# Performance work log

Measured on AMD Instinct MI355X. Metric: run time of the kernel, lower is better.

The kernel has to match this reference:

```python
import jax, jax.numpy as jnp
import numpy as np

B, S, H, NH = 2, 2048, 1024, 16
HD = H // NH  # head_size = 64


def setup_inputs() -> dict:
    key = jax.random.key(0)
    ks = jax.random.split(key, 9)
    sc = 0.02
    return {
        "hidden_states": jax.random.normal(ks[0], (B, S, H), dtype=jnp.float32),
        "Wq": jax.random.normal(ks[1], (H, H), dtype=jnp.float32) * sc,
        "bq": jax.random.normal(ks[2], (H,), dtype=jnp.float32) * sc,
        "Wk": jax.random.normal(ks[3], (H, H), dtype=jnp.float32) * sc,
        "bk": jax.random.normal(ks[4], (H,), dtype=jnp.float32) * sc,
        "Wv": jax.random.normal(ks[5], (H, H), dtype=jnp.float32) * sc,
        "bv": jax.random.normal(ks[6], (H,), dtype=jnp.float32) * sc,
        "Wo": jax.random.normal(ks[7], (H, H), dtype=jnp.float32) * sc,
        "bo": jax.random.normal(ks[8], (H,), dtype=jnp.float32) * sc,
    }


def reference(hidden_states, Wq, bq, Wk, bk, Wv, bv, Wo, bo):
    b, s, h = hidden_states.shape
    # nn.Linear: y = x @ W.T + b
    q = hidden_states @ Wq.T + bq
    k = hidden_states @ Wk.T + bk
    v = hidden_states @ Wv.T + bv
    q = q.reshape(b, s, NH, HD)
    k = k.reshape(b, s, NH, HD)
    v = v.reshape(b, s, NH, HD)
    # scores: [b, heads, q, k]
    scores = jnp.einsum("bqhd,bkhd->bhqk", q, k) / jnp.sqrt(jnp.float32(HD))
    # causal mask: triu(ones, diagonal=1) positions set to -inf
    causal = jnp.triu(jnp.ones((s, s), dtype=bool), k=1)
    scores = jnp.where(causal[None, None], -jnp.inf, scores)
    attn = jax.nn.softmax(scores, axis=-1)
    ctx = jnp.einsum("bhqk,bkhd->bqhd", attn, v).reshape(b, s, h)
    return ctx @ Wo.T + bo
```

## Files before the change

kernel.cpp:

```cpp
#include <hip/hip_runtime.h>
#include <hip/hip_bf16.h>

#define B_  2
#define S_  2048
#define H_  1024
#define NH_ 16
#define HD_ 64

typedef unsigned short u16;
typedef unsigned int   u32;
typedef __attribute__((ext_vector_type(4)))  float  f32x4;
typedef __attribute__((ext_vector_type(16))) float  f32x16;
typedef __attribute__((ext_vector_type(8)))  __bf16 bf16x8;
typedef __attribute__((ext_vector_type(2)))  unsigned int u32x2;
typedef __attribute__((ext_vector_type(4)))  unsigned int u32x4;
typedef __attribute__((ext_vector_type(4)))  unsigned short u16x4;

__device__ __forceinline__ u16 f2bf(float f) {
  unsigned u = __builtin_bit_cast(unsigned, f);
  u += 0x7fffu + ((u >> 16) & 1u);
  return (u16)(u >> 16);
}
__device__ __forceinline__ u32 cvtpk(float lo, float hi) {
  u32 r;
  asm("v_cvt_pk_bf16_f32 %0, %1, %2" : "=v"(r) : "v"(lo), "v"(hi));
  return r;
}
__device__ __forceinline__ float ex2(float x) {
  float r;
  asm("v_exp_f32 %0, %1" : "=v"(r) : "v"(x));
  return r;
}

__device__ __forceinline__ void gload_lds16(const void* g, void* l) {
  __builtin_amdgcn_global_load_lds(
      (const __attribute__((address_space(1))) void*)g,
      (__attribute__((address_space(3))) void*)l, 16, 0, 0);
}

#define NX_ (4u * 1024u * 1024u)
__global__ __launch_bounds__(256) void cvt_all(const float* __restrict__ x,
                                               const float* __restrict__ w0, const float* __restrict__ w1,
                                               const float* __restrict__ w2, const float* __restrict__ w3,
                                               u16* __restrict__ xb,
                                               u16* __restrict__ o0, u16* __restrict__ o1,
                                               u16* __restrict__ o2, u16* __restrict__ o3) {
  size_t i4 = ((size_t)blockIdx.x * 256 + threadIdx.x) * 4;
  const float* src; u16* dst; size_t off;
  if (i4 < (size_t)NX_) { src = x; dst = xb; off = i4; }
  else {
    size_t j = i4 - NX_;
    int seg = (int)(j >> 20);
    off = j & ((1u << 20) - 1);
    src = seg == 0 ? w0 : seg == 1 ? w1 : seg == 2 ? w2 : w3;
    dst = seg == 0 ? o0 : seg == 1 ? o1 : seg == 2 ? o2 : o3;
  }
  float4 v = *reinterpret_cast<const float4*>(src + off);
  u16x4 o;
  o[0] = f2bf(v.x); o[1] = f2bf(v.y); o[2] = f2bf(v.z); o[3] = f2bf(v.w);
  *reinterpret_cast<u16x4*>(dst + off) = o;
}

__device__ __forceinline__ void store_out(float* C, size_t idx, float v) { C[idx] = v; }
__device__ __forceinline__ void store_out(u16* C, size_t idx, float v) { C[idx] = f2bf(v); }

template <int MI, typename OutT>
__device__ __forceinline__ void gemm_core(const u16* __restrict__ A, const u16* __restrict__ Bw,
                                          const float* __restrict__ bias, OutT* __restrict__ C,
                                          int M, int N, int K, float oscale, int m0, int n0,
                                          u16* lsA, u16* lsB) {
  const int t = threadIdx.x;
  const int w = t >> 6, lane = t & 63;
  const int g = lane >> 4, c = lane & 15;
  const int wr = w >> 1, wc = w & 1;

  f32x4 acc[MI][4] = {};
  const int rowS = w * 16 + (lane >> 2);
  const int colS = (lane & 3) * 8;

  for (int k0 = 0; k0 < K; k0 += 32) {
    __syncthreads();
#pragma unroll
    for (int r = 0; r < MI / 2; ++r)
      gload_lds16(A + (size_t)(m0 + r * 64 + rowS) * K + k0 + colS, lsA + r * 2048 + w * 512);
#pragma unroll
    for (int r = 0; r < 2; ++r)
      gload_lds16(Bw + (size_t)(n0 + r * 64 + rowS) * K + k0 + colS, lsB + r * 2048 + w * 512);
    asm volatile("s_waitcnt vmcnt(0)" ::: "memory");
    __syncthreads();

    bf16x8 af[MI], bfr[4];
#pragma unroll
    for (int mi = 0; mi < MI; ++mi)
      af[mi] = *reinterpret_cast<const bf16x8*>(&lsA[(wr * (MI * 16) + mi * 16 + c) * 32 + g * 8]);
#pragma unroll
    for (int ni = 0; ni < 4; ++ni)
      bfr[ni] = *reinterpret_cast<const bf16x8*>(&lsB[(wc * 64 + ni * 16 + c) * 32 + g * 8]);
#pragma unroll
    for (int mi = 0; mi < MI; ++mi)
#pragma unroll
      for (int ni = 0; ni < 4; ++ni)
        acc[mi][ni] = __builtin_amdgcn_mfma_f32_16x16x32_bf16(af[mi], bfr[ni], acc[mi][ni], 0, 0, 0);
  }

#pragma unroll
  for (int mi = 0; mi < MI; ++mi) {
    int rowb = m0 + wr * (MI * 16) + mi * 16 + g * 4;
#pragma unroll
    for (int ni = 0; ni < 4; ++ni) {
      int col = n0 + wc * 64 + ni * 16 + c;
      float bv = bias[col];
#pragma unroll
      for (int r = 0; r < 4; ++r) {
        float v = (acc[mi][ni][r] + bv) * oscale;
        store_out(C, (size_t)(rowb + r) * N + col, v);
      }
    }
  }
}

__global__ __launch_bounds__(256) void gemm_qkv(const u16* __restrict__ xb,
                                                const u16* __restrict__ Wq, const u16* __restrict__ Wk,
                                                const u16* __restrict__ Wv,
                                                const float* __restrict__ bq, const float* __restrict__ bk,
                                                const float* __restrict__ bv,
                                                u16* __restrict__ Q, u16* __restrict__ Kb, u16* __restrict__ Vb,
                                                int M, int K, float qscale) {
  __shared__ u16 lsA[4096];
  __shared__ u16 lsB[4096];
  const int fid = blockIdx.x;
  const int xcd = fid & 7, i = fid >> 3;
  const int mloc = i / 24, nn = i % 24;
  const int m0 = (xcd * 4 + mloc) * 128;
  const int ng = nn * 128;
  const int sel = ng >> 10, n0 = ng & 1023;
  const u16*  W    = sel == 0 ? Wq : sel == 1 ? Wk : Wv;
  const float* bia = sel == 0 ? bq : sel == 1 ? bk : bv;
  u16*        Cp   = sel == 0 ? Q  : sel == 1 ? Kb : Vb;
  float os = sel == 0 ? qscale : 1.0f;
  gemm_core<4, u16>(xb, W, bia, Cp, M, 1024, K, os, m0, n0, lsA, lsB);
}

__global__ __launch_bounds__(256) void gemm_wo(const u16* __restrict__ A, const u16* __restrict__ Bw,
                                               const float* __restrict__ bias, float* __restrict__ C,
                                               int M, int N, int K) {
  __shared__ u16 lsA[2048];
  __shared__ u16 lsB[4096];
  const int fid = blockIdx.x;
  const int xcd = fid & 7, i = fid >> 3;
  const int mloc = i >> 3, nn = i & 7;
  const int m0 = (xcd * 8 + mloc) * 64;
  const int n0 = nn * 128;
  gemm_core<2, float>(A, Bw, bias, C, M, N, K, 1.0f, m0, n0, lsA, lsB);
}

__device__ __forceinline__ void stage_k(const u16* __restrict__ Kg, size_t headoff, int kvb,
                                        int kRow0, int kColB, int w, u16* lsKbuf) {
#pragma unroll
  for (int r = 0; r < 2; ++r)
    gload_lds16((const char*)(Kg + headoff + (size_t)(kvb + r * 32 + kRow0) * H_) + kColB,
                (char*)lsKbuf + r * 4096 + w * 1024);
}

__device__ __forceinline__ void write_vt(u16* dst, const u32x2* va, const u32x2* vb,
                                         int vKv, int vD0, int vS) {
#pragma unroll
  for (int r = 0; r < 2; ++r) {
    int kvx = (r * 32 + vKv) ^ vS;
    u32 w0 = __builtin_amdgcn_perm(vb[r][0], va[r][0], 0x05040100u);
    u32 w1 = __builtin_amdgcn_perm(vb[r][0], va[r][0], 0x07060302u);
    u32 w2 = __builtin_amdgcn_perm(vb[r][1], va[r][1], 0x05040100u);
    u32 w3 = __builtin_amdgcn_perm(vb[r][1], va[r][1], 0x07060302u);
    *reinterpret_cast<u32*>(dst + (vD0 + 0) * 72 + kvx) = w0;
    *reinterpret_cast<u32*>(dst + (vD0 + 1) * 72 + kvx) = w1;
    *reinterpret_cast<u32*>(dst + (vD0 + 2) * 72 + kvx) = w2;
    *reinterpret_cast<u32*>(dst + (vD0 + 3) * 72 + kvx) = w3;
  }
}

__device__ __forceinline__ void pv_sub(const f32x16& sc, float mrun, int ktbase,
                                       const char* vtb, int hi, int c5,
                                       f32x16& o0, f32x16& o1, float& rs) {
  float p[16];
#pragma unroll
  for (int r = 0; r < 16; ++r) p[r] = ex2(sc[r] - mrun);
  rs += ((p[0] + p[1]) + (p[2] + p[3])) + ((p[4] + p[5]) + (p[6] + p[7]))
      + ((p[8] + p[9]) + (p[10] + p[11])) + ((p[12] + p[13]) + (p[14] + p[15]));
  u32 wd[4][2];
#pragma unroll
  for (int a = 0; a < 4; ++a) {
    wd[a][0] = cvtpk(p[4 * a + 0], p[4 * a + 1]);
    wd[a][1] = cvtpk(p[4 * a + 2], p[4 * a + 3]);
  }
#pragma unroll
  for (int ktp = 0; ktp < 2; ++ktp) {
    u32 mw[4];
#pragma unroll
    for (int u = 0; u < 2; ++u) {
      u32 A  = wd[2 * ktp][u], Bv = wd[2 * ktp + 1][u];
      u32 oA = (u32)__shfl_xor((int)A, 32);
      u32 oB = (u32)__shfl_xor((int)Bv, 32);
      mw[u]     = hi ? oB : A;
      mw[2 + u] = hi ? Bv : oA;
    }
    u32x4 pw = {mw[0], mw[1], mw[2], mw[3]};
    bf16x8 pb = __builtin_bit_cast(bf16x8, pw);
    const int kt = ktbase + ktp;
#pragma unroll
    for (int dt = 0; dt < 2; ++dt) {
      int d = 32 * dt + c5;
      int col = (kt * 32 + hi * 16) ^ (16 * ((d >> 3) & 7));
      bf16x8 av = *reinterpret_cast<const bf16x8*>(vtb + d * 144 + col);
      f32x16& oo = dt ? o1 : o0;
      oo = __builtin_amdgcn_mfma_f32_32x32x16_bf16(av, pb, oo, 0, 0, 0);
    }
  }
}

__global__ __launch_bounds__(256, 4) void attn_fwd(const u16* __restrict__ Qg,
                                                   const u16* __restrict__ Kg,
                                                   const u16* __restrict__ Vg,
                                                   u16* __restrict__ Og) {
  __shared__ __align__(16) char smem[34816];
  u16* lsK  = (u16*)smem;
  u16* lsVt = (u16*)(smem + 16384);
  float* lsO  = (float*)smem;
  float* lsML = (float*)(smem + 20480);
  u16*   lsOT = (u16*)(smem + 21504);

  const int blk = blockIdx.x;
  const int xcd = blk & 7, i = blk >> 3;
  const int qt  = 31 - (i >> 2);
  const int bh  = xcd * 4 + (i & 3);
  const int h = bh & 15, b = bh >> 4;

  const int t = threadIdx.x, w = t >> 6, lane = t & 63;
  const int sub = w & 1, par = w >> 1;
  const int c5 = lane & 31, hi = lane >> 5;
  const size_t headoff = (size_t)b * (S_ * H_) + (size_t)h * HD_;
  const int q0w = qt * 64 + 32 * sub;

  const int kO    = w * 1024 + lane * 16;
  const int kRow0 = kO >> 7;
  const int kColB = (kO & 127) ^ ((kRow0 & 7) << 4);
  const int vKv = 2 * (t >> 4);
  const int vD0 = 4 * (t & 15);
  const int vS  = 8 * ((vD0 >> 3) & 7);

  bf16x8 aq[4];
#pragma unroll
  for (int kt = 0; kt < 4; ++kt)
    aq[kt] = *reinterpret_cast<const bf16x8*>(Qg + headoff + (size_t)(q0w + c5) * H_ + kt * 16 + hi * 8);

  f32x16 oacc0 = {}, oacc1 = {};
  float mrun = -1e30f, lrun = 0.f;

  const int NIT = (qt >> 1) + 1;
  for (int n = 0; n < NIT; ++n) {
    const int kvb0 = 2 * n * 64;
    const bool has1 = (2 * n + 1) <= qt;

    u32x2 va0[2], vb0[2], va1[2], vb1[2];
#pragma unroll
    for (int r = 0; r < 2; ++r) {
      const u16* vp = Vg + headoff + (size_t)(kvb0 + r * 32 + vKv) * H_ + vD0;
      va0[r] = *reinterpret_cast<const u32x2*>(vp);
      vb0[r] = *reinterpret_cast<const u32x2*>(vp + H_);
    }
    if (has1) {
#pragma unroll
      for (int r = 0; r < 2; ++r) {
        const u16* vp = Vg + headoff + (size_t)(kvb0 + 64 + r * 32 + vKv) * H_ + vD0;
        va1[r] = *reinterpret_cast<const u32x2*>(vp);
        vb1[r] = *reinterpret_cast<const u32x2*>(vp + H_);
      }
    }
    stage_k(Kg, headoff, kvb0, kRow0, kColB, w, lsK);
    if (has1) stage_k(Kg, headoff, kvb0 + 64, kRow0, kColB, w, lsK + 4096);
    asm volatile("s_waitcnt vmcnt(0)" ::: "memory");
    write_vt(lsVt, va0, vb0, vKv, vD0, vS);
    if (has1) write_vt(lsVt + 4608, va1, vb1, vKv, vD0, vS);
    __syncthreads();

    const int myt = 2 * n + par;
    if (myt <= qt) {
      const char* kb  = (const char*)lsK  + par * 8192;
      const char* vtb = (const char*)lsVt + par * 9216;
      const int nkv = (myt == qt && sub == 0) ? 1 : 2;

      f32x16 sc0 = {}, sc1 = {};
      __builtin_amdgcn_s_setprio(1);
#pragma unroll
      for (int kt = 0; kt < 4; ++kt) {
        int colx = (kt * 32 + hi * 16) ^ ((c5 & 7) << 4);
        bf16x8 ak0 = *reinterpret_cast<const bf16x8*>(kb + c5 * 128 + colx);
        sc0 = __builtin_amdgcn_mfma_f32_32x32x16_bf16(ak0, aq[kt], sc0, 0, 0, 0);
      }
      if (nkv == 2) {
#pragma unroll
        for (int kt = 0; kt < 4; ++kt) {
          int colx = (kt * 32 + hi * 16) ^ ((c5 & 7) << 4);
          bf16x8 ak1 = *reinterpret_cast<const bf16x8*>(kb + (32 + c5) * 128 + colx);
          sc1 = __builtin_amdgcn_mfma_f32_32x32x16_bf16(ak1, aq[kt], sc1, 0, 0, 0);
        }
      }
      __builtin_amdgcn_s_setprio(0);

      if (myt == qt) {
        const int qg = q0w + c5;
#pragma unroll
        for (int r = 0; r < 16; ++r) {
          int kvg = myt * 64 + (r & 3) + 8 * (r >> 2) + 4 * hi;
          sc0[r] = (kvg > qg) ? -1e30f : sc0[r];
          if (nkv == 2) sc1[r] = (kvg + 32 > qg) ? -1e30f : sc1[r];
        }
      }

      float pm = sc0[0];
#pragma unroll
      for (int r = 1; r < 16; ++r) pm = fmaxf(pm, sc0[r]);
      if (nkv == 2) {
#pragma unroll
        for (int r = 0; r < 16; ++r) pm = fmaxf(pm, sc1[r]);
      }
      pm = fmaxf(pm, (float)__shfl_xor(pm, 32));

      if (!__all(pm <= mrun + 8.0f)) {
        float mn = fmaxf(mrun, pm);
        float s8 = ex2(mrun - mn);
        mrun = mn; lrun *= s8;
#pragma unroll
        for (int r = 0; r < 16; ++r) { oacc0[r] *= s8; oacc1[r] *= s8; }
      }

      float rs = 0.f;
      pv_sub(sc0, mrun, 0, vtb, hi, c5, oacc0, oacc1, rs);
      if (nkv == 2) pv_sub(sc1, mrun, 2, vtb, hi, c5, oacc0, oacc1, rs);
      rs += (float)__shfl_xor(rs, 32);
      lrun += rs;
    }
    __syncthreads();
  }

  if (par == 0) {
    if (hi == 0) { lsML[sub * 64 + c5] = mrun; lsML[sub * 64 + 32 + c5] = lrun; }
#pragma unroll
    for (int dt = 0; dt < 2; ++dt) {
      float* dst = lsO + ((size_t)((sub * 2 + dt) * 64 + lane)) * 20;
      const f32x16& oo = dt ? oacc1 : oacc0;
#pragma unroll
      for (int k4 = 0; k4 < 4; ++k4) {
        f32x4 v4 = {oo[4 * k4], oo[4 * k4 + 1], oo[4 * k4 + 2], oo[4 * k4 + 3]};
        *reinterpret_cast<f32x4*>(dst + 4 * k4) = v4;
      }
    }
  }
  __syncthreads();
  if (par == 1) {
    float mA = lsML[sub * 64 + c5];
    float lA = lsML[sub * 64 + 32 + c5];
    float mn = fmaxf(mA, mrun);
    float sA = ex2(mA - mn), sB = ex2(mrun - mn);
    float linv = 1.0f / (lA * sA + lrun * sB);
    sA *= linv; sB *= linv;
    u16* ot = lsOT + sub * 32 * 72;
#pragma unroll
    for (int dt = 0; dt < 2; ++dt) {
      const float* sp = lsO + ((size_t)((sub * 2 + dt) * 64 + lane)) * 20;
      f32x4 a4[4];
#pragma unroll
      for (int k4 = 0; k4 < 4; ++k4) a4[k4] = *reinterpret_cast<const f32x4*>(sp + 4 * k4);
      const f32x16& oo = dt ? oacc1 : oacc0;
#pragma unroll
      for (int a = 0; a < 4; ++a)
#pragma unroll
        for (int u = 0; u < 2; ++u) {
          int r = 4 * a + 2 * u;
          float o0 = a4[a][2 * u]     * sA + oo[r]     * sB;
          float o1 = a4[a][2 * u + 1] * sA + oo[r + 1] * sB;
          int d = 32 * dt + 8 * a + 4 * hi + 2 * u;
          *reinterpret_cast<u32*>(ot + c5 * 72 + d) = cvtpk(o0, o1);
        }
    }
    asm volatile("s_waitcnt lgkmcnt(0)" ::: "memory");
    __builtin_amdgcn_sched_barrier(0);
#pragma unroll
    for (int rr = 0; rr < 4; ++rr) {
      int q = 8 * rr + (lane >> 3);
      int d8 = (lane & 7) * 8;
      u32x4 vv = *reinterpret_cast<const u32x4*>(ot + q * 72 + d8);
      *reinterpret_cast<u32x4*>(Og + headoff + (size_t)(qt * 64 + 32 * sub + q) * H_ + d8) = vv;
    }
  }
}

extern "C" void kernel_launch(void* const* d_in, const int* in_sizes, int n_in,
                              void* d_out, int out_size, void* d_ws, size_t ws_size,
                              hipStream_t stream) {
  const float* x  = (const float*)d_in[0];
  const float* Wq = (const float*)d_in[1];
  const float* bq = (const float*)d_in[2];
  const float* Wk = (const float*)d_in[3];
  const float* bk = (const float*)d_in[4];
  const float* Wv = (const float*)d_in[5];
  const float* bv = (const float*)d_in[6];
  const float* Wo = (const float*)d_in[7];
  const float* bo = (const float*)d_in[8];
  float* out = (float*)d_out;

  const size_t MT = (size_t)B_ * S_;
  char* p = (char*)d_ws;
  u16* xb  = (u16*)p; p += MT * H_ * 2;
  u16* Wqb = (u16*)p; p += (size_t)H_ * H_ * 2;
  u16* Wkb = (u16*)p; p += (size_t)H_ * H_ * 2;
  u16* Wvb = (u16*)p; p += (size_t)H_ * H_ * 2;
  u16* Wob = (u16*)p; p += (size_t)H_ * H_ * 2;
  u16* Qb  = (u16*)p; p += MT * H_ * 2;
  u16* Kb  = (u16*)p; p += MT * H_ * 2;
  u16* Vb  = (u16*)p; p += MT * H_ * 2;
  u16* Cb  = xb;

  cvt_all<<<8192, 256, 0, stream>>>(x, Wq, Wk, Wv, Wo, xb, Wqb, Wkb, Wvb, Wob);

  const float qscale = 0.125f * 1.44269504088896f;
  gemm_qkv<<<768, 256, 0, stream>>>(xb, Wqb, Wkb, Wvb, bq, bk, bv,
                                    Qb, Kb, Vb, (int)MT, H_, qscale);

  attn_fwd<<<1024, 256, 0, stream>>>(Qb, Kb, Vb, Cb);

  gemm_wo<<<512, 256, 0, stream>>>(Cb, Wob, bo, out, (int)MT, H_, H_);
}
```

Measured before the change: 113.2 us.

## Restructure attention to 128-query tiles with double-buffered K/V prefetch

```diff
diff --git a/kernel.cpp b/kernel.cpp
--- a/kernel.cpp
+++ b/kernel.cpp
@@ -162,6 +162,16 @@
                 (char*)lsKbuf + r * 4096 + w * 1024);
 }
 
+__device__ __forceinline__ void load_v(const u16* __restrict__ Vg, size_t headoff, int kvb,
+                                       int vKv, int vD0, u32x2* va, u32x2* vb) {
+#pragma unroll
+  for (int r = 0; r < 2; ++r) {
+    const u16* vp = Vg + headoff + (size_t)(kvb + r * 32 + vKv) * H_ + vD0;
+    va[r] = *reinterpret_cast<const u32x2*>(vp);
+    vb[r] = *reinterpret_cast<const u32x2*>(vp + H_);
+  }
+}
+
 __device__ __forceinline__ void write_vt(u16* dst, const u32x2* va, const u32x2* vb,
                                          int vKv, int vD0, int vS) {
 #pragma unroll
@@ -224,21 +234,21 @@
   __shared__ __align__(16) char smem[34816];
   u16* lsK  = (u16*)smem;
   u16* lsVt = (u16*)(smem + 16384);
-  float* lsO  = (float*)smem;
-  float* lsML = (float*)(smem + 20480);
-  u16*   lsOT = (u16*)(smem + 21504);
+  u16* lsOT = (u16*)smem;
 
   const int blk = blockIdx.x;
   const int xcd = blk & 7, i = blk >> 3;
-  const int qt  = 31 - (i >> 2);
+  const int qt  = 15 - (i >> 2);
   const int bh  = xcd * 4 + (i & 3);
   const int h = bh & 15, b = bh >> 4;
 
   const int t = threadIdx.x, w = t >> 6, lane = t & 63;
-  const int sub = w & 1, par = w >> 1;
   const int c5 = lane & 31, hi = lane >> 5;
   const size_t headoff = (size_t)b * (S_ * H_) + (size_t)h * HD_;
-  const int q0w = qt * 64 + 32 * sub;
+  const int q0w = qt * 128 + 32 * w;
+  const int NT  = 2 * qt + 2;
+  const int ktd = q0w >> 6;
+  const bool evenAligned = ((q0w & 63) == 0);
 
   const int kO    = w * 1024 + lane * 16;
   const int kRow0 = kO >> 7;
@@ -249,74 +259,60 @@
 
   bf16x8 aq[4];
 #pragma unroll
-  for (int kt = 0; kt < 4; ++kt)
-    aq[kt] = *reinterpret_cast<const bf16x8*>(Qg + headoff + (size_t)(q0w + c5) * H_ + kt * 16 + hi * 8);
+  for (int kc = 0; kc < 4; ++kc)
+    aq[kc] = *reinterpret_cast<const bf16x8*>(Qg + headoff + (size_t)(q0w + c5) * H_ + kc * 16 + hi * 8);
 
   f32x16 oacc0 = {}, oacc1 = {};
   float mrun = -1e30f, lrun = 0.f;
-
-  const int NIT = (qt >> 1) + 1;
-  for (int n = 0; n < NIT; ++n) {
-    const int kvb0 = 2 * n * 64;
-    const bool has1 = (2 * n + 1) <= qt;
-
-    u32x2 va0[2], vb0[2], va1[2], vb1[2];
-#pragma unroll
-    for (int r = 0; r < 2; ++r) {
-      const u16* vp = Vg + headoff + (size_t)(kvb0 + r * 32 + vKv) * H_ + vD0;
-      va0[r] = *reinterpret_cast<const u32x2*>(vp);
-      vb0[r] = *reinterpret_cast<const u32x2*>(vp + H_);
-    }
-    if (has1) {
-#pragma unroll
-      for (int r = 0; r < 2; ++r) {
-        const u16* vp = Vg + headoff + (size_t)(kvb0 + 64 + r * 32 + vKv) * H_ + vD0;
-        va1[r] = *reinterpret_cast<const u32x2*>(vp);
-        vb1[r] = *reinterpret_cast<const u32x2*>(vp + H_);
-      }
-    }
-    stage_k(Kg, headoff, kvb0, kRow0, kColB, w, lsK);
-    if (has1) stage_k(Kg, headoff, kvb0 + 64, kRow0, kColB, w, lsK + 4096);
-    asm volatile("s_waitcnt vmcnt(0)" ::: "memory");
-    write_vt(lsVt, va0, vb0, vKv, vD0, vS);
-    if (has1) write_vt(lsVt + 4608, va1, vb1, vKv, vD0, vS);
-    __syncthreads();
-
-    const int myt = 2 * n + par;
-    if (myt <= qt) {
-      const char* kb  = (const char*)lsK  + par * 8192;
-      const char* vtb = (const char*)lsVt + par * 9216;
-      const int nkv = (myt == qt && sub == 0) ? 1 : 2;
-
-      f32x16 sc0 = {}, sc1 = {};
+  u32x2 va[2], vb[2];
+
+  load_v(Vg, headoff, 0, vKv, vD0, va, vb);
+  stage_k(Kg, headoff, 0, kRow0, kColB, w, lsK);
+  asm volatile("s_waitcnt vmcnt(2)" ::: "memory");
+  write_vt(lsVt, va, vb, vKv, vD0, vS);
+  __syncthreads();
+
+  for (int it = 0; it < NT; ++it) {
+    const int cur = it & 1;
+    const bool st = (it + 1 < NT);
+    if (st) {
+      load_v(Vg, headoff, (it + 1) * 64, vKv, vD0, va, vb);
+      stage_k(Kg, headoff, (it + 1) * 64, kRow0, kColB, w, lsK + (cur ^ 1) * 4096);
+    }
+
+    const bool live = (it <= ktd);
+    const int nkv = (it == ktd && evenAligned) ? 1 : 2;
+    f32x16 sc0 = {}, sc1 = {};
+    float pm = -1e30f;
+    if (live) {
+      const char* kb = (const char*)(lsK + cur * 4096);
       __builtin_amdgcn_s_setprio(1);
 #pragma unroll
-      for (int kt = 0; kt < 4; ++kt) {
-        int colx = (kt * 32 + hi * 16) ^ ((c5 & 7) << 4);
+      for (int kc = 0; kc < 4; ++kc) {
+        int colx = (kc * 32 + hi * 16) ^ ((c5 & 7) << 4);
         bf16x8 ak0 = *reinterpret_cast<const bf16x8*>(kb + c5 * 128 + colx);
-        sc0 = __builtin_amdgcn_mfma_f32_32x32x16_bf16(ak0, aq[kt], sc0, 0, 0, 0);
+        sc0 = __builtin_amdgcn_mfma_f32_32x32x16_bf16(ak0, aq[kc], sc0, 0, 0, 0);
       }
       if (nkv == 2) {
 #pragma unroll
-        for (int kt = 0; kt < 4; ++kt) {
-          int colx = (kt * 32 + hi * 16) ^ ((c5 & 7) << 4);
+        for (int kc = 0; kc < 4; ++kc) {
+          int colx = (kc * 32 + hi * 16) ^ ((c5 & 7) << 4);
           bf16x8 ak1 = *reinterpret_cast<const bf16x8*>(kb + (32 + c5) * 128 + colx);
-          sc1 = __builtin_amdgcn_mfma_f32_32x32x16_bf16(ak1, aq[kt], sc1, 0, 0, 0);
+          sc1 = __builtin_amdgcn_mfma_f32_32x32x16_bf16(ak1, aq[kc], sc1, 0, 0, 0);
         }
       }
       __builtin_amdgcn_s_setprio(0);
 
-      if (myt == qt) {
-        const int qg = q0w + c5;
+      if (it == ktd) {
 #pragma unroll
         for (int r = 0; r < 16; ++r) {
-          int kvg = myt * 64 + (r & 3) + 8 * (r >> 2) + 4 * hi;
-          sc0[r] = (kvg > qg) ? -1e30f : sc0[r];
-          if (nkv == 2) sc1[r] = (kvg + 32 > qg) ? -1e30f : sc1[r];
+          int j = (r & 3) + 8 * (r >> 2) + 4 * hi;
+          if (evenAligned) sc0[r] = (j > c5) ? -1e30f : sc0[r];
+          else             sc1[r] = (j > c5) ? -1e30f : sc1[r];
         }
       }
 
-      float pm = sc0[0];
+      pm = sc0[0];
 #pragma unroll
       for (int r = 1; r < 16; ++r) pm = fmaxf(pm, sc0[r]);
       if (nkv == 2) {
@@ -332,65 +328,50 @@
 #pragma unroll
         for (int r = 0; r < 16; ++r) { oacc0[r] *= s8; oacc1[r] *= s8; }
       }
-
+    }
+
+    if (st) {
+      asm volatile("s_waitcnt vmcnt(2)" ::: "memory");
+      write_vt(lsVt + (cur ^ 1) * 4608, va, vb, vKv, vD0, vS);
+    }
+
+    if (live) {
+      const char* vtb = (const char*)(lsVt + cur * 4608);
       float rs = 0.f;
+      __builtin_amdgcn_s_setprio(1);
       pv_sub(sc0, mrun, 0, vtb, hi, c5, oacc0, oacc1, rs);
       if (nkv == 2) pv_sub(sc1, mrun, 2, vtb, hi, c5, oacc0, oacc1, rs);
+      __builtin_amdgcn_s_setprio(0);
       rs += (float)__shfl_xor(rs, 32);
       lrun += rs;
     }
+
     __syncthreads();
   }
 
-  if (par == 0) {
-    if (hi == 0) { lsML[sub * 64 + c5] = mrun; lsML[sub * 64 + 32 + c5] = lrun; }
-#pragma unroll
-    for (int dt = 0; dt < 2; ++dt) {
-      float* dst = lsO + ((size_t)((sub * 2 + dt) * 64 + lane)) * 20;
-      const f32x16& oo = dt ? oacc1 : oacc0;
-#pragma unroll
-      for (int k4 = 0; k4 < 4; ++k4) {
-        f32x4 v4 = {oo[4 * k4], oo[4 * k4 + 1], oo[4 * k4 + 2], oo[4 * k4 + 3]};
-        *reinterpret_cast<f32x4*>(dst + 4 * k4) = v4;
-      }
-    }
-  }
-  __syncthreads();
-  if (par == 1) {
-    float mA = lsML[sub * 64 + c5];
-    float lA = lsML[sub * 64 + 32 + c5];
-    float mn = fmaxf(mA, mrun);
-    float sA = ex2(mA - mn), sB = ex2(mrun - mn);
-    float linv = 1.0f / (lA * sA + lrun * sB);
-    sA *= linv; sB *= linv;
-    u16* ot = lsOT + sub * 32 * 72;
-#pragma unroll
-    for (int dt = 0; dt < 2; ++dt) {
-      const float* sp = lsO + ((size_t)((sub * 2 + dt) * 64 + lane)) * 20;
-      f32x4 a4[4];
-#pragma unroll
-      for (int k4 = 0; k4 < 4; ++k4) a4[k4] = *reinterpret_cast<const f32x4*>(sp + 4 * k4);
-      const f32x16& oo = dt ? oacc1 : oacc0;
-#pragma unroll
-      for (int a = 0; a < 4; ++a)
-#pragma unroll
-        for (int u = 0; u < 2; ++u) {
-          int r = 4 * a + 2 * u;
-          float o0 = a4[a][2 * u]     * sA + oo[r]     * sB;
-          float o1 = a4[a][2 * u + 1] * sA + oo[r + 1] * sB;
-          int d = 32 * dt + 8 * a + 4 * hi + 2 * u;
-          *reinterpret_cast<u32*>(ot + c5 * 72 + d) = cvtpk(o0, o1);
-        }
-    }
-    asm volatile("s_waitcnt lgkmcnt(0)" ::: "memory");
-    __builtin_amdgcn_sched_barrier(0);
-#pragma unroll
-    for (int rr = 0; rr < 4; ++rr) {
-      int q = 8 * rr + (lane >> 3);
-      int d8 = (lane & 7) * 8;
-      u32x4 vv = *reinterpret_cast<const u32x4*>(ot + q * 72 + d8);
-      *reinterpret_cast<u32x4*>(Og + headoff + (size_t)(qt * 64 + 32 * sub + q) * H_ + d8) = vv;
-    }
+  float linv = 1.0f / lrun;
+  u16* ot = lsOT + w * 2304;
+#pragma unroll
+  for (int dt = 0; dt < 2; ++dt) {
+    const f32x16& oo = dt ? oacc1 : oacc0;
+#pragma unroll
+    for (int a = 0; a < 4; ++a)
+#pragma unroll
+      for (int u = 0; u < 2; ++u) {
+        int r = 4 * a + 2 * u;
+        float o0 = oo[r] * linv, o1 = oo[r + 1] * linv;
+        int d = 32 * dt + 8 * a + 4 * hi + 2 * u;
+        *reinterpret_cast<u32*>(ot + c5 * 72 + d) = cvtpk(o0, o1);
+      }
+  }
+  asm volatile("s_waitcnt lgkmcnt(0)" ::: "memory");
+  __builtin_amdgcn_sched_barrier(0);
+#pragma unroll
+  for (int rr = 0; rr < 4; ++rr) {
+    int q = 8 * rr + (lane >> 3);
+    int d8 = (lane & 7) * 8;
+    u32x4 vv = *reinterpret_cast<const u32x4*>(ot + q * 72 + d8);
+    *reinterpret_cast<u32x4*>(Og + headoff + (size_t)(q0w + q) * H_ + d8) = vv;
   }
 }
 
@@ -426,7 +407,7 @@
   gemm_qkv<<<768, 256, 0, stream>>>(xb, Wqb, Wkb, Wvb, bq, bk, bv,
                                     Qb, Kb, Vb, (int)MT, H_, qscale);
 
-  attn_fwd<<<1024, 256, 0, stream>>>(Qb, Kb, Vb, Cb);
+  attn_fwd<<<512, 256, 0, stream>>>(Qb, Kb, Vb, Cb);
 
   gemm_wo<<<512, 256, 0, stream>>>(Cb, Wob, bo, out, (int)MT, H_, H_);
 }
```

After: 147.1 us. 29.9% more time.

## Double-buffer attention K/V tiles and deepen GEMM K-step to 64

Applied to the files above, without the earlier changes.

```diff
diff --git a/kernel.cpp b/kernel.cpp
--- a/kernel.cpp
+++ b/kernel.cpp
@@ -12,7 +12,6 @@
 typedef __attribute__((ext_vector_type(4)))  float  f32x4;
 typedef __attribute__((ext_vector_type(16))) float  f32x16;
 typedef __attribute__((ext_vector_type(8)))  __bf16 bf16x8;
-typedef __attribute__((ext_vector_type(2)))  unsigned int u32x2;
 typedef __attribute__((ext_vector_type(4)))  unsigned int u32x4;
 typedef __attribute__((ext_vector_type(4)))  unsigned short u16x4;
 
@@ -73,34 +72,45 @@
   const int w = t >> 6, lane = t & 63;
   const int g = lane >> 4, c = lane & 15;
   const int wr = w >> 1, wc = w & 1;
+  const int srow = lane >> 3;
+  const int scol = (lane & 7) * 8;
 
   f32x4 acc[MI][4] = {};
-  const int rowS = w * 16 + (lane >> 2);
-  const int colS = (lane & 3) * 8;
-
-  for (int k0 = 0; k0 < K; k0 += 32) {
+
+  for (int k0 = 0; k0 < K; k0 += 64) {
     __syncthreads();
 #pragma unroll
-    for (int r = 0; r < MI / 2; ++r)
-      gload_lds16(A + (size_t)(m0 + r * 64 + rowS) * K + k0 + colS, lsA + r * 2048 + w * 512);
-#pragma unroll
-    for (int r = 0; r < 2; ++r)
-      gload_lds16(Bw + (size_t)(n0 + r * 64 + rowS) * K + k0 + colS, lsB + r * 2048 + w * 512);
+    for (int j = 0; j < MI; ++j)
+      gload_lds16(A + (size_t)(m0 + 8 * (w * MI + j) + srow) * K + k0 + scol,
+                  lsA + 8 * (w * MI + j) * 64 + lane * 8);
+#pragma unroll
+    for (int j = 0; j < 4; ++j)
+      gload_lds16(Bw + (size_t)(n0 + 8 * (w * 4 + j) + srow) * K + k0 + scol,
+                  lsB + 8 * (w * 4 + j) * 64 + lane * 8);
     asm volatile("s_waitcnt vmcnt(0)" ::: "memory");
     __syncthreads();
 
-    bf16x8 af[MI], bfr[4];
+    bf16x8 af[MI][2], bfr[4][2];
 #pragma unroll
     for (int mi = 0; mi < MI; ++mi)
-      af[mi] = *reinterpret_cast<const bf16x8*>(&lsA[(wr * (MI * 16) + mi * 16 + c) * 32 + g * 8]);
+#pragma unroll
+      for (int kh = 0; kh < 2; ++kh)
+        af[mi][kh] = *reinterpret_cast<const bf16x8*>(
+            &lsA[(wr * (MI * 16) + mi * 16 + c) * 64 + kh * 32 + g * 8]);
 #pragma unroll
     for (int ni = 0; ni < 4; ++ni)
-      bfr[ni] = *reinterpret_cast<const bf16x8*>(&lsB[(wc * 64 + ni * 16 + c) * 32 + g * 8]);
-#pragma unroll
-    for (int mi = 0; mi < MI; ++mi)
-#pragma unroll
-      for (int ni = 0; ni < 4; ++ni)
-        acc[mi][ni] = __builtin_amdgcn_mfma_f32_16x16x32_bf16(af[mi], bfr[ni], acc[mi][ni], 0, 0, 0);
+#pragma unroll
+      for (int kh = 0; kh < 2; ++kh)
+        bfr[ni][kh] = *reinterpret_cast<const bf16x8*>(
+            &lsB[(wc * 64 + ni * 16 + c) * 64 + kh * 32 + g * 8]);
+#pragma unroll
+    for (int kh = 0; kh < 2; ++kh)
+#pragma unroll
+      for (int mi = 0; mi < MI; ++mi)
+#pragma unroll
+        for (int ni = 0; ni < 4; ++ni)
+          acc[mi][ni] = __builtin_amdgcn_mfma_f32_16x16x32_bf16(af[mi][kh], bfr[ni][kh],
+                                                                acc[mi][ni], 0, 0, 0);
   }
 
 #pragma unroll
@@ -126,8 +136,8 @@
                                                 const float* __restrict__ bv,
                                                 u16* __restrict__ Q, u16* __restrict__ Kb, u16* __restrict__ Vb,
                                                 int M, int K, float qscale) {
-  __shared__ u16 lsA[4096];
-  __shared__ u16 lsB[4096];
+  __shared__ u16 lsA[8192];
+  __shared__ u16 lsB[8192];
   const int fid = blockIdx.x;
   const int xcd = fid & 7, i = fid >> 3;
   const int mloc = i / 24, nn = i % 24;
@@ -144,8 +154,8 @@
 __global__ __launch_bounds__(256) void gemm_wo(const u16* __restrict__ A, const u16* __restrict__ Bw,
                                                const float* __restrict__ bias, float* __restrict__ C,
                                                int M, int N, int K) {
-  __shared__ u16 lsA[2048];
-  __shared__ u16 lsB[4096];
+  __shared__ u16 lsA[4096];
+  __shared__ u16 lsB[8192];
   const int fid = blockIdx.x;
   const int xcd = fid & 7, i = fid >> 3;
   const int mloc = i >> 3, nn = i & 7;
@@ -154,192 +164,167 @@
   gemm_core<2, float>(A, Bw, bias, C, M, N, K, 1.0f, m0, n0, lsA, lsB);
 }
 
-__device__ __forceinline__ void stage_k(const u16* __restrict__ Kg, size_t headoff, int kvb,
-                                        int kRow0, int kColB, int w, u16* lsKbuf) {
-#pragma unroll
-  for (int r = 0; r < 2; ++r)
-    gload_lds16((const char*)(Kg + headoff + (size_t)(kvb + r * 32 + kRow0) * H_) + kColB,
-                (char*)lsKbuf + r * 4096 + w * 1024);
-}
-
-__device__ __forceinline__ void write_vt(u16* dst, const u32x2* va, const u32x2* vb,
-                                         int vKv, int vD0, int vS) {
-#pragma unroll
-  for (int r = 0; r < 2; ++r) {
-    int kvx = (r * 32 + vKv) ^ vS;
-    u32 w0 = __builtin_amdgcn_perm(vb[r][0], va[r][0], 0x05040100u);
-    u32 w1 = __builtin_amdgcn_perm(vb[r][0], va[r][0], 0x07060302u);
-    u32 w2 = __builtin_amdgcn_perm(vb[r][1], va[r][1], 0x05040100u);
-    u32 w3 = __builtin_amdgcn_perm(vb[r][1], va[r][1], 0x07060302u);
-    *reinterpret_cast<u32*>(dst + (vD0 + 0) * 72 + kvx) = w0;
-    *reinterpret_cast<u32*>(dst + (vD0 + 1) * 72 + kvx) = w1;
-    *reinterpret_cast<u32*>(dst + (vD0 + 2) * 72 + kvx) = w2;
-    *reinterpret_cast<u32*>(dst + (vD0 + 3) * 72 + kvx) = w3;
-  }
-}
-
-__device__ __forceinline__ void pv_sub(const f32x16& sc, float mrun, int ktbase,
-                                       const char* vtb, int hi, int c5,
-                                       f32x16& o0, f32x16& o1, float& rs) {
-  float p[16];
-#pragma unroll
-  for (int r = 0; r < 16; ++r) p[r] = ex2(sc[r] - mrun);
-  rs += ((p[0] + p[1]) + (p[2] + p[3])) + ((p[4] + p[5]) + (p[6] + p[7]))
-      + ((p[8] + p[9]) + (p[10] + p[11])) + ((p[12] + p[13]) + (p[14] + p[15]));
-  u32 wd[4][2];
-#pragma unroll
-  for (int a = 0; a < 4; ++a) {
-    wd[a][0] = cvtpk(p[4 * a + 0], p[4 * a + 1]);
-    wd[a][1] = cvtpk(p[4 * a + 2], p[4 * a + 3]);
-  }
-#pragma unroll
-  for (int ktp = 0; ktp < 2; ++ktp) {
-    u32 mw[4];
-#pragma unroll
-    for (int u = 0; u < 2; ++u) {
-      u32 A  = wd[2 * ktp][u], Bv = wd[2 * ktp + 1][u];
-      u32 oA = (u32)__shfl_xor((int)A, 32);
-      u32 oB = (u32)__shfl_xor((int)Bv, 32);
-      mw[u]     = hi ? oB : A;
-      mw[2 + u] = hi ? Bv : oA;
-    }
-    u32x4 pw = {mw[0], mw[1], mw[2], mw[3]};
-    bf16x8 pb = __builtin_bit_cast(bf16x8, pw);
-    const int kt = ktbase + ktp;
-#pragma unroll
-    for (int dt = 0; dt < 2; ++dt) {
-      int d = 32 * dt + c5;
-      int col = (kt * 32 + hi * 16) ^ (16 * ((d >> 3) & 7));
-      bf16x8 av = *reinterpret_cast<const bf16x8*>(vtb + d * 144 + col);
-      f32x16& oo = dt ? o1 : o0;
-      oo = __builtin_amdgcn_mfma_f32_32x32x16_bf16(av, pb, oo, 0, 0, 0);
-    }
-  }
-}
-
 __global__ __launch_bounds__(256, 4) void attn_fwd(const u16* __restrict__ Qg,
                                                    const u16* __restrict__ Kg,
                                                    const u16* __restrict__ Vg,
                                                    u16* __restrict__ Og) {
-  __shared__ __align__(16) char smem[34816];
-  u16* lsK  = (u16*)smem;
-  u16* lsVt = (u16*)(smem + 16384);
+  __shared__ __align__(16) u16 smem[18432];
+  u16* lsKb = smem;
+  u16* lsVb = smem + 8192;
   float* lsO  = (float*)smem;
-  float* lsML = (float*)(smem + 20480);
-  u16*   lsOT = (u16*)(smem + 21504);
+  float* lsML = (float*)((char*)smem + 20480);
+  u16*   lsOT = smem + 10752;
 
   const int blk = blockIdx.x;
   const int xcd = blk & 7, i = blk >> 3;
-  const int qt  = 31 - (i >> 2);
-  const int bh  = xcd * 4 + (i & 3);
+  const int j5 = i & 31, bgrp = i >> 5;
+  const int qt = 31 - ((j5 + 8 * bgrp) & 31);
+  const int bh = xcd * 4 + bgrp;
   const int h = bh & 15, b = bh >> 4;
 
   const int t = threadIdx.x, w = t >> 6, lane = t & 63;
+  const int c5 = lane & 31, hi = lane >> 5;
   const int sub = w & 1, par = w >> 1;
-  const int c5 = lane & 31, hi = lane >> 5;
   const size_t headoff = (size_t)b * (S_ * H_) + (size_t)h * HD_;
   const int q0w = qt * 64 + 32 * sub;
 
-  const int kO    = w * 1024 + lane * 16;
-  const int kRow0 = kO >> 7;
-  const int kColB = (kO & 127) ^ ((kRow0 & 7) << 4);
-  const int vKv = 2 * (t >> 4);
-  const int vD0 = 4 * (t & 15);
-  const int vS  = 8 * ((vD0 >> 3) & 7);
+  const int sp = w & 1, sh = w >> 1;
+  const int kRowLoc = 16 * sh + (lane >> 3);
+  const int kSrcCol = ((lane & 7) ^ (lane >> 3)) << 4;
+  const int vKvLoc  = 16 * sh + 2 * (lane >> 3);
+  const int vD0     = 8 * (lane & 7);
+  const int vKvx    = vKvLoc ^ (((lane & 7) & 3) << 3);
+
+  int qkOff[4];
+#pragma unroll
+  for (int kc = 0; kc < 4; ++kc)
+    qkOff[kc] = c5 * 128 + ((32 * kc + 16 * hi) ^ ((c5 & 7) << 4));
+  const int pvRow0 = c5 * 80, pvRow1 = (32 + c5) * 80;
+  int pvCol[2];
+#pragma unroll
+  for (int kp2 = 0; kp2 < 2; ++kp2)
+    pvCol[kp2] = 2 * ((16 * kp2 + 8 * hi) ^ ((c5 >> 3) << 3));
 
   bf16x8 aq[4];
 #pragma unroll
-  for (int kt = 0; kt < 4; ++kt)
-    aq[kt] = *reinterpret_cast<const bf16x8*>(Qg + headoff + (size_t)(q0w + c5) * H_ + kt * 16 + hi * 8);
-
-  f32x16 oacc0 = {}, oacc1 = {};
+  for (int kc = 0; kc < 4; ++kc)
+    aq[kc] = *reinterpret_cast<const bf16x8*>(Qg + headoff + (size_t)(q0w + c5) * H_ + kc * 16 + hi * 8);
+
+  f32x16 o0 = {}, o1 = {};
   float mrun = -1e30f, lrun = 0.f;
-
-  const int NIT = (qt >> 1) + 1;
-  for (int n = 0; n < NIT; ++n) {
-    const int kvb0 = 2 * n * 64;
-    const bool has1 = (2 * n + 1) <= qt;
-
-    u32x2 va0[2], vb0[2], va1[2], vb1[2];
-#pragma unroll
-    for (int r = 0; r < 2; ++r) {
-      const u16* vp = Vg + headoff + (size_t)(kvb0 + r * 32 + vKv) * H_ + vD0;
-      va0[r] = *reinterpret_cast<const u32x2*>(vp);
-      vb0[r] = *reinterpret_cast<const u32x2*>(vp + H_);
-    }
-    if (has1) {
-#pragma unroll
-      for (int r = 0; r < 2; ++r) {
-        const u16* vp = Vg + headoff + (size_t)(kvb0 + 64 + r * 32 + vKv) * H_ + vD0;
-        va1[r] = *reinterpret_cast<const u32x2*>(vp);
-        vb1[r] = *reinterpret_cast<const u32x2*>(vp + H_);
-      }
-    }
-    stage_k(Kg, headoff, kvb0, kRow0, kColB, w, lsK);
-    if (has1) stage_k(Kg, headoff, kvb0 + 64, kRow0, kColB, w, lsK + 4096);
-    asm volatile("s_waitcnt vmcnt(0)" ::: "memory");
-    write_vt(lsVt, va0, vb0, vKv, vD0, vS);
-    if (has1) write_vt(lsVt + 4608, va1, vb1, vKv, vD0, vS);
-    __syncthreads();
-
-    const int myt = 2 * n + par;
-    if (myt <= qt) {
-      const char* kb  = (const char*)lsK  + par * 8192;
-      const char* vtb = (const char*)lsVt + par * 9216;
-      const int nkv = (myt == qt && sub == 0) ? 1 : 2;
-
-      f32x16 sc0 = {}, sc1 = {};
+  u32x4 vA, vB;
+
+  auto STAGE = [&](int m) {
+    const int kv0 = m * 64 + 32 * sp;
+    const u16* vp = Vg + headoff + (size_t)(kv0 + vKvLoc) * H_ + vD0;
+    vA = *reinterpret_cast<const u32x4*>(vp);
+    vB = *reinterpret_cast<const u32x4*>(vp + H_);
+    char* kt = (char*)(lsKb + ((m & 1) * 2 + sp) * 2048) + 16 * sh * 128;
+    const char* ks = (const char*)(Kg + headoff + (size_t)(kv0 + kRowLoc) * H_) + kSrcCol;
+    gload_lds16(ks, kt);
+    gload_lds16(ks + 8 * (H_ * 2), kt + 8 * 128);
+  };
+  auto WRITEVT = [&](int m) {
+    u16* vt = lsVb + ((m & 1) * 2 + sp) * 2560;
+#pragma unroll
+    for (int jj = 0; jj < 4; ++jj) {
+      u32 lo  = __builtin_amdgcn_perm(vB[jj], vA[jj], 0x05040100u);
+      u32 hi2 = __builtin_amdgcn_perm(vB[jj], vA[jj], 0x07060302u);
+      *reinterpret_cast<u32*>(vt + (vD0 + 2 * jj) * 40 + vKvx)     = lo;
+      *reinterpret_cast<u32*>(vt + (vD0 + 2 * jj + 1) * 40 + vKvx) = hi2;
+    }
+  };
+
+  STAGE(0);
+  asm volatile("s_waitcnt vmcnt(2)" ::: "memory");
+  WRITEVT(0);
+  asm volatile("s_waitcnt lgkmcnt(0)" ::: "memory");
+  asm volatile("s_waitcnt vmcnt(0)" ::: "memory");
+  __builtin_amdgcn_s_barrier();
+
+  for (int n = 0; n <= qt; ++n) {
+    const int buf = n & 1;
+    const bool st = n < qt;
+    if (st) STAGE(n + 1);
+
+    const bool live = (2 * n + par) <= (2 * qt + sub);
+    const bool diag = (2 * n + par) == (2 * qt + sub);
+    f32x16 sc = {};
+    if (live) {
+      const char* kb = (const char*)(lsKb + (buf * 2 + par) * 2048);
       __builtin_amdgcn_s_setprio(1);
 #pragma unroll
-      for (int kt = 0; kt < 4; ++kt) {
-        int colx = (kt * 32 + hi * 16) ^ ((c5 & 7) << 4);
-        bf16x8 ak0 = *reinterpret_cast<const bf16x8*>(kb + c5 * 128 + colx);
-        sc0 = __builtin_amdgcn_mfma_f32_32x32x16_bf16(ak0, aq[kt], sc0, 0, 0, 0);
-      }
-      if (nkv == 2) {
-#pragma unroll
-        for (int kt = 0; kt < 4; ++kt) {
-          int colx = (kt * 32 + hi * 16) ^ ((c5 & 7) << 4);
-          bf16x8 ak1 = *reinterpret_cast<const bf16x8*>(kb + (32 + c5) * 128 + colx);
-          sc1 = __builtin_amdgcn_mfma_f32_32x32x16_bf16(ak1, aq[kt], sc1, 0, 0, 0);
+      for (int kc = 0; kc < 4; ++kc) {
+        bf16x8 ak = *reinterpret_cast<const bf16x8*>(kb + qkOff[kc]);
+        sc = __builtin_amdgcn_mfma_f32_32x32x16_bf16(ak, aq[kc], sc, 0, 0, 0);
+      }
+      __builtin_amdgcn_s_setprio(0);
+      if (diag) {
+#pragma unroll
+        for (int r = 0; r < 16; ++r) {
+          int kvl = (r & 3) + 8 * (r >> 2) + 4 * hi;
+          sc[r] = (kvl > c5) ? -1e30f : sc[r];
         }
       }
-      __builtin_amdgcn_s_setprio(0);
-
-      if (myt == qt) {
-        const int qg = q0w + c5;
-#pragma unroll
-        for (int r = 0; r < 16; ++r) {
-          int kvg = myt * 64 + (r & 3) + 8 * (r >> 2) + 4 * hi;
-          sc0[r] = (kvg > qg) ? -1e30f : sc0[r];
-          if (nkv == 2) sc1[r] = (kvg + 32 > qg) ? -1e30f : sc1[r];
-        }
-      }
-
-      float pm = sc0[0];
-#pragma unroll
-      for (int r = 1; r < 16; ++r) pm = fmaxf(pm, sc0[r]);
-      if (nkv == 2) {
-#pragma unroll
-        for (int r = 0; r < 16; ++r) pm = fmaxf(pm, sc1[r]);
-      }
+      float pm = sc[0];
+#pragma unroll
+      for (int r = 1; r < 16; ++r) pm = fmaxf(pm, sc[r]);
       pm = fmaxf(pm, (float)__shfl_xor(pm, 32));
-
       if (!__all(pm <= mrun + 8.0f)) {
         float mn = fmaxf(mrun, pm);
         float s8 = ex2(mrun - mn);
         mrun = mn; lrun *= s8;
 #pragma unroll
-        for (int r = 0; r < 16; ++r) { oacc0[r] *= s8; oacc1[r] *= s8; }
-      }
-
+        for (int r = 0; r < 16; ++r) { o0[r] *= s8; o1[r] *= s8; }
+      }
+    }
+
+    if (st) {
+      asm volatile("s_waitcnt vmcnt(2)" ::: "memory");
+      WRITEVT(n + 1);
+    }
+
+    if (live) {
+      const char* vtb = (const char*)(lsVb + (buf * 2 + par) * 2560);
       float rs = 0.f;
-      pv_sub(sc0, mrun, 0, vtb, hi, c5, oacc0, oacc1, rs);
-      if (nkv == 2) pv_sub(sc1, mrun, 2, vtb, hi, c5, oacc0, oacc1, rs);
+      u32 wd0[2], wd1[2], wd2[2], wd3[2];
+#pragma unroll
+      for (int a = 0; a < 4; ++a) {
+        float p0 = ex2(sc[4 * a + 0] - mrun), p1 = ex2(sc[4 * a + 1] - mrun);
+        float p2 = ex2(sc[4 * a + 2] - mrun), p3 = ex2(sc[4 * a + 3] - mrun);
+        rs += (p0 + p1) + (p2 + p3);
+        u32* wdp = a == 0 ? wd0 : a == 1 ? wd1 : a == 2 ? wd2 : wd3;
+        wdp[0] = cvtpk(p0, p1);
+        wdp[1] = cvtpk(p2, p3);
+      }
       rs += (float)__shfl_xor(rs, 32);
       lrun += rs;
-    }
-    __syncthreads();
+      __builtin_amdgcn_s_setprio(1);
+#pragma unroll
+      for (int kp2 = 0; kp2 < 2; ++kp2) {
+        u32 wa0 = kp2 ? wd2[0] : wd0[0], wa1 = kp2 ? wd2[1] : wd0[1];
+        u32 wb0 = kp2 ? wd3[0] : wd1[0], wb1 = kp2 ? wd3[1] : wd1[1];
+        u32 own0 = hi ? wb0 : wa0, own1 = hi ? wb1 : wa1;
+        u32 snd0 = hi ? wa0 : wb0, snd1 = hi ? wa1 : wb1;
+        u32 oth0 = (u32)__shfl_xor((int)snd0, 32);
+        u32 oth1 = (u32)__shfl_xor((int)snd1, 32);
+        u32x4 pw;
+        pw[0] = hi ? oth0 : own0;
+        pw[1] = hi ? oth1 : own1;
+        pw[2] = hi ? own0 : oth0;
+        pw[3] = hi ? own1 : oth1;
+        bf16x8 pb = __builtin_bit_cast(bf16x8, pw);
+        bf16x8 av0 = *reinterpret_cast<const bf16x8*>(vtb + pvRow0 + pvCol[kp2]);
+        bf16x8 av1 = *reinterpret_cast<const bf16x8*>(vtb + pvRow1 + pvCol[kp2]);
+        o0 = __builtin_amdgcn_mfma_f32_32x32x16_bf16(av0, pb, o0, 0, 0, 0);
+        o1 = __builtin_amdgcn_mfma_f32_32x32x16_bf16(av1, pb, o1, 0, 0, 0);
+      }
+      __builtin_amdgcn_s_setprio(0);
+    }
+
+    asm volatile("s_waitcnt lgkmcnt(0)" ::: "memory");
+    if (st) asm volatile("s_waitcnt vmcnt(0)" ::: "memory");
+    __builtin_amdgcn_s_barrier();
   }
 
   if (par == 0) {
@@ -347,7 +332,7 @@
 #pragma unroll
     for (int dt = 0; dt < 2; ++dt) {
       float* dst = lsO + ((size_t)((sub * 2 + dt) * 64 + lane)) * 20;
-      const f32x16& oo = dt ? oacc1 : oacc0;
+      const f32x16& oo = dt ? o1 : o0;
 #pragma unroll
       for (int k4 = 0; k4 < 4; ++k4) {
         f32x4 v4 = {oo[4 * k4], oo[4 * k4 + 1], oo[4 * k4 + 2], oo[4 * k4 + 3]};
@@ -363,23 +348,23 @@
     float sA = ex2(mA - mn), sB = ex2(mrun - mn);
     float linv = 1.0f / (lA * sA + lrun * sB);
     sA *= linv; sB *= linv;
-    u16* ot = lsOT + sub * 32 * 72;
+    u16* ot = lsOT + sub * 2304;
 #pragma unroll
     for (int dt = 0; dt < 2; ++dt) {
-      const float* sp = lsO + ((size_t)((sub * 2 + dt) * 64 + lane)) * 20;
+      const float* sp2 = lsO + ((size_t)((sub * 2 + dt) * 64 + lane)) * 20;
       f32x4 a4[4];
 #pragma unroll
-      for (int k4 = 0; k4 < 4; ++k4) a4[k4] = *reinterpret_cast<const f32x4*>(sp + 4 * k4);
-      const f32x16& oo = dt ? oacc1 : oacc0;
+      for (int k4 = 0; k4 < 4; ++k4) a4[k4] = *reinterpret_cast<const f32x4*>(sp2 + 4 * k4);
+      const f32x16& oo = dt ? o1 : o0;
 #pragma unroll
       for (int a = 0; a < 4; ++a)
 #pragma unroll
         for (int u = 0; u < 2; ++u) {
           int r = 4 * a + 2 * u;
-          float o0 = a4[a][2 * u]     * sA + oo[r]     * sB;
-          float o1 = a4[a][2 * u + 1] * sA + oo[r + 1] * sB;
+          float e0 = a4[a][2 * u]     * sA + oo[r]     * sB;
+          float e1 = a4[a][2 * u + 1] * sA + oo[r + 1] * sB;
           int d = 32 * dt + 8 * a + 4 * hi + 2 * u;
-          *reinterpret_cast<u32*>(ot + c5 * 72 + d) = cvtpk(o0, o1);
+          *reinterpret_cast<u32*>(ot + c5 * 72 + d) = cvtpk(e0, e1);
         }
     }
     asm volatile("s_waitcnt lgkmcnt(0)" ::: "memory");
```

New measurement: 133.0 us. 1.17x slower.
